# Performance work log

Measured on AMD Instinct MI355X. Metric: run time of the kernel, lower is better.

## Reference

```python
import jax, jax.numpy as jnp
import numpy as np


def _up(x, h, w):
    # bicubic (Keys a=-0.5, matching PIL BICUBIC) resize of [B,H,W] -> [B,h,w]
    return jax.image.resize(x, (x.shape[0], h, w), method='cubic')


def setup_inputs() -> dict:
    key = jax.random.key(0)
    ks = jax.random.split(key, 10)
    B = 64
    inp = {
        'cam_256': jax.random.uniform(ks[0], (B, 256, 256), dtype=jnp.float32),
        'cam_128': jax.random.uniform(ks[1], (B, 128, 128), dtype=jnp.float32),
        'cam_64':  jax.random.uniform(ks[2], (B, 64, 64), dtype=jnp.float32),
        'cam_32':  jax.random.uniform(ks[3], (B, 32, 32), dtype=jnp.float32),
        'w1': jax.random.normal(ks[4], (2,), dtype=jnp.float32),
        'b1': jax.random.normal(ks[5], (1,), dtype=jnp.float32),
        'w2': jax.random.normal(ks[6], (2,), dtype=jnp.float32),
        'b2': jax.random.normal(ks[7], (1,), dtype=jnp.float32),
        'w3': jax.random.normal(ks[8], (2,), dtype=jnp.float32),
        'b3': jax.random.normal(ks[9], (1,), dtype=jnp.float32),
    }
    return inp


def reference(cam_256, cam_128, cam_64, cam_32, w1, b1, w2, b2, w3, b3):
    B = cam_32.shape[0]
    # stage 1: up(32->64), concat with cam_64, 1x1 conv(2->1) + ReLU
    up32 = _up(cam_32, 64, 64)                              # [B,64,64]
    h64 = jax.nn.relu(w1[0] * up32 + w1[1] * cam_64 + b1[0])
    # stage 2: up(64->128), concat with cam_128, 1x1 conv + ReLU
    up64 = _up(h64, 128, 128)
    h128 = jax.nn.relu(w2[0] * up64 + w2[1] * cam_128 + b2[0])
    # stage 3: up(128->256), concat with cam_256, 1x1 conv + ReLU
    up128 = _up(h128, 256, 256)
    h256 = jax.nn.relu(w3[0] * up128 + w3[1] * cam_256 + b3[0])
    # final: bicubic up to 1024; original loop prepends each new image,
    # reversing batch order -> replicate with flip
    out = _up(h256, 1024, 1024)                             # [B,1024,1024]
    out = jnp.flip(out, axis=0)[:, None]                    # [B,1,1024,1024]
    return out
```

## Files before the change

kernel.cpp:

```cpp
#include <hip/hip_runtime.h>

typedef float vfloat4 __attribute__((ext_vector_type(4)));

__device__ __forceinline__ int iclamp(int v, int lo, int hi) {
  return v < lo ? lo : (v > hi ? hi : v);
}

__device__ __forceinline__ void taps4w(int i, int n, float inv, float w[4]) {
  float s = ((float)i + 0.5f) * inv - 0.5f;
  int k0 = (int)floorf(s);
  float sum = 0.f;
#pragma unroll
  for (int t = 0; t < 4; ++t) {
    int j = k0 - 1 + t;
    float d = fabsf(s - (float)j);
    float wt = (d <= 1.f) ? (((1.5f * d - 2.5f) * d) * d + 1.f)
                          : (((-0.5f * d + 2.5f) * d - 4.f) * d + 2.f);
    if (j < 0 || j >= n) wt = 0.f;
    w[t] = wt;
    sum += wt;
  }
  float r = 1.f / sum;
#pragma unroll
  for (int t = 0; t < 4; ++t) w[t] *= r;
}

#define W0_0 (-0.0439453125f)
#define W0_1 ( 0.3896484375f)
#define W0_2 ( 0.7275390625f)
#define W0_3 (-0.0732421875f)
#define W1_0 (-0.0068359375f)
#define W1_1 ( 0.0908203125f)
#define W1_2 ( 0.9638671875f)
#define W1_3 (-0.0478515625f)
#define U_0 (-0.0234375f)
#define U_1 ( 0.2265625f)
#define U_2 ( 0.8671875f)
#define U_3 (-0.0703125f)

__device__ __forceinline__ void up2_cell(const float (&f)[5][5], int k, int g, int n,
                                         float (&o)[2][2]) {
  if (g >= 2 && g <= n - 3 && k >= 2 && k <= n - 3) {
    float v0[5], v1[5];
#pragma unroll
    for (int c = 0; c < 5; ++c) {
      v0[c] = U_0 * f[0][c] + U_1 * f[1][c] + U_2 * f[2][c] + U_3 * f[3][c];
      v1[c] = U_3 * f[1][c] + U_2 * f[2][c] + U_1 * f[3][c] + U_0 * f[4][c];
    }
    o[0][0] = U_0 * v0[0] + U_1 * v0[1] + U_2 * v0[2] + U_3 * v0[3];
    o[0][1] = U_3 * v0[1] + U_2 * v0[2] + U_1 * v0[3] + U_0 * v0[4];
    o[1][0] = U_0 * v1[0] + U_1 * v1[1] + U_2 * v1[2] + U_3 * v1[3];
    o[1][1] = U_3 * v1[1] + U_2 * v1[2] + U_1 * v1[3] + U_0 * v1[4];
  } else {
#pragma unroll
    for (int p = 0; p < 2; ++p) {
      float wy[4];
      taps4w(2 * k + p, n, 0.5f, wy);
      float vv[5];
#pragma unroll
      for (int c = 0; c < 5; ++c)
        vv[c] = wy[0] * f[p][c] + wy[1] * f[p + 1][c] + wy[2] * f[p + 2][c] + wy[3] * f[p + 3][c];
#pragma unroll
      for (int q = 0; q < 2; ++q) {
        float wx[4];
        taps4w(2 * g + q, n, 0.5f, wx);
        o[p][q] = wx[0] * vv[q] + wx[1] * vv[q + 1] + wx[2] * vv[q + 2] + wx[3] * vv[q + 3];
      }
    }
  }
}

__device__ __forceinline__ void up4_cell(const float (&f)[5][5], int k, int g, int n,
                                         float (&o)[4][4]) {
  if (g >= 2 && g <= n - 3 && k >= 2 && k <= n - 3) {
    float vy[4][5];
#pragma unroll
    for (int c = 0; c < 5; ++c) {
      vy[0][c] = W0_0 * f[0][c] + W0_1 * f[1][c] + W0_2 * f[2][c] + W0_3 * f[3][c];
      vy[1][c] = W1_0 * f[0][c] + W1_1 * f[1][c] + W1_2 * f[2][c] + W1_3 * f[3][c];
      vy[2][c] = W1_3 * f[1][c] + W1_2 * f[2][c] + W1_1 * f[3][c] + W1_0 * f[4][c];
      vy[3][c] = W0_3 * f[1][c] + W0_2 * f[2][c] + W0_1 * f[3][c] + W0_0 * f[4][c];
    }
#pragma unroll
    for (int p = 0; p < 4; ++p) {
      o[p][0] = W0_0 * vy[p][0] + W0_1 * vy[p][1] + W0_2 * vy[p][2] + W0_3 * vy[p][3];
      o[p][1] = W1_0 * vy[p][0] + W1_1 * vy[p][1] + W1_2 * vy[p][2] + W1_3 * vy[p][3];
      o[p][2] = W1_3 * vy[p][1] + W1_2 * vy[p][2] + W1_1 * vy[p][3] + W1_0 * vy[p][4];
      o[p][3] = W0_3 * vy[p][1] + W0_2 * vy[p][2] + W0_1 * vy[p][3] + W0_0 * vy[p][4];
    }
  } else {
#pragma unroll
    for (int p = 0; p < 4; ++p) {
      float wy[4];
      taps4w(4 * k + p, n, 0.25f, wy);
      int oy = (p < 2) ? 0 : 1;
      float vv[5];
#pragma unroll
      for (int c = 0; c < 5; ++c)
        vv[c] = wy[0] * f[oy][c] + wy[1] * f[oy + 1][c] + wy[2] * f[oy + 2][c] + wy[3] * f[oy + 3][c];
#pragma unroll
      for (int q = 0; q < 4; ++q) {
        float wx[4];
        taps4w(4 * g + q, n, 0.25f, wx);
        int ox = (q < 2) ? 0 : 1;
        o[p][q] = wx[0] * vv[ox] + wx[1] * vv[ox + 1] + wx[2] * vv[ox + 2] + wx[3] * vv[ox + 3];
      }
    }
  }
}

__global__ void __launch_bounds__(512, 4) fused_all(
    const float* __restrict__ cam256, const float* __restrict__ cam128,
    const float* __restrict__ cam64, const float* __restrict__ cam32,
    const float* __restrict__ w1, const float* __restrict__ b1,
    const float* __restrict__ w2, const float* __restrict__ b2,
    const float* __restrict__ w3, const float* __restrict__ b3,
    float* __restrict__ out) {
  __shared__ float s_h64[16 * 64];
  __shared__ float s_h128[24 * 128];
  __shared__ float s_h256[36 * 256];

  const int tid = threadIdx.x;
  const int slab = blockIdx.x;
  const int b = blockIdx.y;
  const int s = slab * 32;

  const int r_lo = s - 2 < 0 ? 0 : s - 2, r_hi = s + 33 > 255 ? 255 : s + 33;
  const int kr0 = r_lo >> 1, kr1 = r_hi >> 1;
  const int h256_row0 = 2 * kr0;
  const int j_lo = kr0 - 2 < 0 ? 0 : kr0 - 2, j_hi = kr1 + 2 > 127 ? 127 : kr1 + 2;
  const int kj0 = j_lo >> 1, kj1 = j_hi >> 1;
  const int h128_row0 = 2 * kj0;
  const int m_lo = kj0 - 2 < 0 ? 0 : kj0 - 2, m_hi = kj1 + 2 > 63 ? 63 : kj1 + 2;
  const int km0 = m_lo >> 1, km1 = m_hi >> 1;
  const int h64_row0 = 2 * km0;

  const float w1_0 = w1[0], w1_1 = w1[1], b1_0 = b1[0];
  const float w2_0 = w2[0], w2_1 = w2[1], b2_0 = b2[0];
  const float w3_0 = w3[0], w3_1 = w3[1], b3_0 = b3[0];

  {
    const float* c32 = cam32 + (size_t)b * 32 * 32;
    const float* c64 = cam64 + (size_t)b * 64 * 64;
    const int nk = km1 - km0 + 1;
    for (int idx = tid; idx < nk * 32; idx += 512) {
      int k = km0 + (idx >> 5), g = idx & 31;
      float f[5][5];
#pragma unroll
      for (int i = 0; i < 5; ++i) {
        int r = iclamp(k - 2 + i, 0, 31);
#pragma unroll
        for (int c = 0; c < 5; ++c) f[i][c] = c32[r * 32 + iclamp(g - 2 + c, 0, 31)];
      }
      float o[2][2];
      up2_cell(f, k, g, 32, o);
#pragma unroll
      for (int p = 0; p < 2; ++p)
#pragma unroll
        for (int q = 0; q < 2; ++q) {
          int row = 2 * k + p, col = 2 * g + q;
          float h = w1_0 * o[p][q] + w1_1 * c64[row * 64 + col] + b1_0;
          s_h64[(row - h64_row0) * 64 + col] = fmaxf(h, 0.f);
        }
    }
  }
  __syncthreads();

  {
    const float* c128 = cam128 + (size_t)b * 128 * 128;
    const int nk = kj1 - kj0 + 1;
    for (int idx = tid; idx < nk * 64; idx += 512) {
      int k = kj0 + (idx >> 6), g = idx & 63;
      float f[5][5];
#pragma unroll
      for (int i = 0; i < 5; ++i) {
        int r = iclamp(k - 2 + i, 0, 63) - h64_row0;
#pragma unroll
        for (int c = 0; c < 5; ++c) f[i][c] = s_h64[r * 64 + iclamp(g - 2 + c, 0, 63)];
      }
      float o[2][2];
      up2_cell(f, k, g, 64, o);
#pragma unroll
      for (int p = 0; p < 2; ++p)
#pragma unroll
        for (int q = 0; q < 2; ++q) {
          int row = 2 * k + p, col = 2 * g + q;
          float h = w2_0 * o[p][q] + w2_1 * c128[row * 128 + col] + b2_0;
          s_h128[(row - h128_row0) * 128 + col] = fmaxf(h, 0.f);
        }
    }
  }
  __syncthreads();

  {
    const float* c256 = cam256 + (size_t)b * 256 * 256;
    const int nk = kr1 - kr0 + 1;
    for (int idx = tid; idx < nk * 128; idx += 512) {
      int k = kr0 + (idx >> 7), g = idx & 127;
      float f[5][5];
#pragma unroll
      for (int i = 0; i < 5; ++i) {
        int r = iclamp(k - 2 + i, 0, 127) - h128_row0;
#pragma unroll
        for (int c = 0; c < 5; ++c) f[i][c] = s_h128[r * 128 + iclamp(g - 2 + c, 0, 127)];
      }
      float o[2][2];
      up2_cell(f, k, g, 128, o);
#pragma unroll
      for (int p = 0; p < 2; ++p)
#pragma unroll
        for (int q = 0; q < 2; ++q) {
          int row = 2 * k + p, col = 2 * g + q;
          float h = w3_0 * o[p][q] + w3_1 * c256[row * 256 + col] + b3_0;
          s_h256[(row - h256_row0) * 256 + col] = fmaxf(h, 0.f);
        }
    }
  }
  __syncthreads();

  {
    float* outimg = out + (size_t)(63 - b) * 1024 * 1024;
    for (int idx = tid; idx < 32 * 256; idx += 512) {
      int k = s + (idx >> 8), g = idx & 255;
      float f[5][5];
#pragma unroll
      for (int i = 0; i < 5; ++i) {
        int r = iclamp(k - 2 + i, 0, 255) - h256_row0;
#pragma unroll
        for (int c = 0; c < 5; ++c) f[i][c] = s_h256[r * 256 + iclamp(g - 2 + c, 0, 255)];
      }
      float o[4][4];
      up4_cell(f, k, g, 256, o);
#pragma unroll
      for (int p = 0; p < 4; ++p) {
        vfloat4 v = {o[p][0], o[p][1], o[p][2], o[p][3]};
        __builtin_nontemporal_store(v, (vfloat4*)(outimg + (size_t)(4 * k + p) * 1024 + 4 * g));
      }
    }
  }
}

extern "C" void kernel_launch(void* const* d_in, const int* in_sizes, int n_in_,
                              void* d_out, int out_size, void* d_ws, size_t ws_size,
                              hipStream_t stream) {
  const float* cam256 = (const float*)d_in[0];
  const float* cam128 = (const float*)d_in[1];
  const float* cam64  = (const float*)d_in[2];
  const float* cam32  = (const float*)d_in[3];
  const float* w1 = (const float*)d_in[4];
  const float* b1 = (const float*)d_in[5];
  const float* w2 = (const float*)d_in[6];
  const float* b2 = (const float*)d_in[7];
  const float* w3 = (const float*)d_in[8];
  const float* b3 = (const float*)d_in[9];
  float* out = (float*)d_out;

  fused_all<<<dim3(8, 64), 512, 0, stream>>>(cam256, cam128, cam64, cam32,
                                             w1, b1, w2, b2, w3, b3, out);
}
```

Measured before the change: 334.5 us.

## Use sliding-window separable passes with register reuse in final two upsample stages

Stage 3 and the final 4x upsample now give each thread a fixed column and a run of consecutive rows. Each new row's horizontal filter result is kept in a 5-row register window that shifts down one row per step, so every shared-memory row is loaded and filtered horizontally once rather than five times. Column tap weights are computed once per thread, and stage 3 uses float2 loads and stores. The trade-off is more registers per thread and serial per-thread row loops, which may lower occupancy or reduce parallelism.

```diff
diff --git a/kernel.cpp b/kernel.cpp
--- a/kernel.cpp
+++ b/kernel.cpp
@@ -1,6 +1,7 @@
 #include <hip/hip_runtime.h>
 
 typedef float vfloat4 __attribute__((ext_vector_type(4)));
+typedef float vfloat2 __attribute__((ext_vector_type(2)));
 
 __device__ __forceinline__ int iclamp(int v, int lo, int hi) {
   return v < lo ? lo : (v > hi ? hi : v);
@@ -70,45 +71,6 @@
   }
 }
 
-__device__ __forceinline__ void up4_cell(const float (&f)[5][5], int k, int g, int n,
-                                         float (&o)[4][4]) {
-  if (g >= 2 && g <= n - 3 && k >= 2 && k <= n - 3) {
-    float vy[4][5];
-#pragma unroll
-    for (int c = 0; c < 5; ++c) {
-      vy[0][c] = W0_0 * f[0][c] + W0_1 * f[1][c] + W0_2 * f[2][c] + W0_3 * f[3][c];
-      vy[1][c] = W1_0 * f[0][c] + W1_1 * f[1][c] + W1_2 * f[2][c] + W1_3 * f[3][c];
-      vy[2][c] = W1_3 * f[1][c] + W1_2 * f[2][c] + W1_1 * f[3][c] + W1_0 * f[4][c];
-      vy[3][c] = W0_3 * f[1][c] + W0_2 * f[2][c] + W0_1 * f[3][c] + W0_0 * f[4][c];
-    }
-#pragma unroll
-    for (int p = 0; p < 4; ++p) {
-      o[p][0] = W0_0 * vy[p][0] + W0_1 * vy[p][1] + W0_2 * vy[p][2] + W0_3 * vy[p][3];
-      o[p][1] = W1_0 * vy[p][0] + W1_1 * vy[p][1] + W1_2 * vy[p][2] + W1_3 * vy[p][3];
-      o[p][2] = W1_3 * vy[p][1] + W1_2 * vy[p][2] + W1_1 * vy[p][3] + W1_0 * vy[p][4];
-      o[p][3] = W0_3 * vy[p][1] + W0_2 * vy[p][2] + W0_1 * vy[p][3] + W0_0 * vy[p][4];
-    }
-  } else {
-#pragma unroll
-    for (int p = 0; p < 4; ++p) {
-      float wy[4];
-      taps4w(4 * k + p, n, 0.25f, wy);
-      int oy = (p < 2) ? 0 : 1;
-      float vv[5];
-#pragma unroll
-      for (int c = 0; c < 5; ++c)
-        vv[c] = wy[0] * f[oy][c] + wy[1] * f[oy + 1][c] + wy[2] * f[oy + 2][c] + wy[3] * f[oy + 3][c];
-#pragma unroll
-      for (int q = 0; q < 4; ++q) {
-        float wx[4];
-        taps4w(4 * g + q, n, 0.25f, wx);
-        int ox = (q < 2) ? 0 : 1;
-        o[p][q] = wx[0] * vv[ox] + wx[1] * vv[ox + 1] + wx[2] * vv[ox + 2] + wx[3] * vv[ox + 3];
-      }
-    }
-  }
-}
-
 __global__ void __launch_bounds__(512, 4) fused_all(
     const float* __restrict__ cam256, const float* __restrict__ cam128,
     const float* __restrict__ cam64, const float* __restrict__ cam32,
@@ -194,49 +156,155 @@
 
   {
     const float* c256 = cam256 + (size_t)b * 256 * 256;
+    const int gc = tid & 127;
+    const int sub = tid >> 7;
     const int nk = kr1 - kr0 + 1;
-    for (int idx = tid; idx < nk * 128; idx += 512) {
-      int k = kr0 + (idx >> 7), g = idx & 127;
-      float f[5][5];
-#pragma unroll
-      for (int i = 0; i < 5; ++i) {
-        int r = iclamp(k - 2 + i, 0, 127) - h128_row0;
-#pragma unroll
-        for (int c = 0; c < 5; ++c) f[i][c] = s_h128[r * 128 + iclamp(g - 2 + c, 0, 127)];
-      }
-      float o[2][2];
-      up2_cell(f, k, g, 128, o);
-#pragma unroll
-      for (int p = 0; p < 2; ++p)
-#pragma unroll
-        for (int q = 0; q < 2; ++q) {
-          int row = 2 * k + p, col = 2 * g + q;
-          float h = w3_0 * o[p][q] + w3_1 * c256[row * 256 + col] + b3_0;
-          s_h256[(row - h256_row0) * 256 + col] = fmaxf(h, 0.f);
+    const int len = (nk + 3) >> 2;
+    const int ks = kr0 + sub * len;
+    int ke = ks + len - 1;
+    if (ke > kr1) ke = kr1;
+    if (ks <= kr1) {
+      const int cc0 = iclamp(gc - 2, 0, 127), cc1 = iclamp(gc - 1, 0, 127), cc2 = gc,
+                cc3 = iclamp(gc + 1, 0, 127), cc4 = iclamp(gc + 2, 0, 127);
+      float wa0, wa1, wa2, wa3, wb0, wb1, wb2, wb3;
+      if (gc >= 2 && gc <= 125) {
+        wa0 = U_0; wa1 = U_1; wa2 = U_2; wa3 = U_3;
+        wb0 = U_3; wb1 = U_2; wb2 = U_1; wb3 = U_0;
+      } else {
+        float ta[4], tb[4];
+        taps4w(2 * gc, 128, 0.5f, ta);
+        taps4w(2 * gc + 1, 128, 0.5f, tb);
+        wa0 = ta[0]; wa1 = ta[1]; wa2 = ta[2]; wa3 = ta[3];
+        wb0 = tb[0]; wb1 = tb[1]; wb2 = tb[2]; wb3 = tb[3];
+      }
+#define H128_ROW_HX(RCLAMP, DST)                                                \
+      {                                                                         \
+        const float* rp_ = s_h128 + ((RCLAMP) - h128_row0) * 128;               \
+        float f0_ = rp_[cc0], f1_ = rp_[cc1], f2_ = rp_[cc2], f3_ = rp_[cc3],   \
+              f4_ = rp_[cc4];                                                   \
+        DST[0] = wa0 * f0_ + wa1 * f1_ + wa2 * f2_ + wa3 * f3_;                 \
+        DST[1] = wb0 * f1_ + wb1 * f2_ + wb2 * f3_ + wb3 * f4_;                 \
+      }
+      float hx[5][2];
+#pragma unroll
+      for (int w = 0; w < 5; ++w) {
+        int rc = iclamp(ks - 2 + w, 0, 127);
+        H128_ROW_HX(rc, hx[w]);
+      }
+      for (int k = ks; k <= ke; ++k) {
+        if (k > ks) {
+#pragma unroll
+          for (int w = 0; w < 4; ++w) { hx[w][0] = hx[w + 1][0]; hx[w][1] = hx[w + 1][1]; }
+          int rc = iclamp(k + 2, 0, 127);
+          H128_ROW_HX(rc, hx[4]);
         }
+        float p0w[4], p1w[4];
+        if (k < 2 || k > 125) {
+          taps4w(2 * k, 128, 0.5f, p0w);
+          taps4w(2 * k + 1, 128, 0.5f, p1w);
+        } else {
+          p0w[0] = U_0; p0w[1] = U_1; p0w[2] = U_2; p0w[3] = U_3;
+          p1w[0] = U_3; p1w[1] = U_2; p1w[2] = U_1; p1w[3] = U_0;
+        }
+        float o00 = p0w[0] * hx[0][0] + p0w[1] * hx[1][0] + p0w[2] * hx[2][0] + p0w[3] * hx[3][0];
+        float o01 = p0w[0] * hx[0][1] + p0w[1] * hx[1][1] + p0w[2] * hx[2][1] + p0w[3] * hx[3][1];
+        float o10 = p1w[0] * hx[1][0] + p1w[1] * hx[2][0] + p1w[2] * hx[3][0] + p1w[3] * hx[4][0];
+        float o11 = p1w[0] * hx[1][1] + p1w[1] * hx[2][1] + p1w[2] * hx[3][1] + p1w[3] * hx[4][1];
+        const int row0 = 2 * k, col = 2 * gc;
+        vfloat2 ca = *(const vfloat2*)(c256 + (size_t)row0 * 256 + col);
+        vfloat2 cb = *(const vfloat2*)(c256 + (size_t)(row0 + 1) * 256 + col);
+        vfloat2 h0 = {fmaxf(w3_0 * o00 + w3_1 * ca.x + b3_0, 0.f),
+                      fmaxf(w3_0 * o01 + w3_1 * ca.y + b3_0, 0.f)};
+        vfloat2 h1 = {fmaxf(w3_0 * o10 + w3_1 * cb.x + b3_0, 0.f),
+                      fmaxf(w3_0 * o11 + w3_1 * cb.y + b3_0, 0.f)};
+        *(vfloat2*)(&s_h256[(row0 - h256_row0) * 256 + col]) = h0;
+        *(vfloat2*)(&s_h256[(row0 + 1 - h256_row0) * 256 + col]) = h1;
+      }
+#undef H128_ROW_HX
     }
   }
   __syncthreads();
 
   {
     float* outimg = out + (size_t)(63 - b) * 1024 * 1024;
-    for (int idx = tid; idx < 32 * 256; idx += 512) {
-      int k = s + (idx >> 8), g = idx & 255;
-      float f[5][5];
-#pragma unroll
-      for (int i = 0; i < 5; ++i) {
-        int r = iclamp(k - 2 + i, 0, 255) - h256_row0;
-#pragma unroll
-        for (int c = 0; c < 5; ++c) f[i][c] = s_h256[r * 256 + iclamp(g - 2 + c, 0, 255)];
-      }
-      float o[4][4];
-      up4_cell(f, k, g, 256, o);
-#pragma unroll
-      for (int p = 0; p < 4; ++p) {
-        vfloat4 v = {o[p][0], o[p][1], o[p][2], o[p][3]};
-        __builtin_nontemporal_store(v, (vfloat4*)(outimg + (size_t)(4 * k + p) * 1024 + 4 * g));
-      }
-    }
+    const int g = tid & 255;
+    const int kbase = s + (tid >> 8) * 16;
+    const int cc0 = iclamp(g - 2, 0, 255), cc1 = iclamp(g - 1, 0, 255), cc2 = g,
+              cc3 = iclamp(g + 1, 0, 255), cc4 = iclamp(g + 2, 0, 255);
+    float wx00, wx01, wx02, wx03, wx10, wx11, wx12, wx13;
+    float wx20, wx21, wx22, wx23, wx30, wx31, wx32, wx33;
+    if (g >= 2 && g <= 253) {
+      wx00 = W0_0; wx01 = W0_1; wx02 = W0_2; wx03 = W0_3;
+      wx10 = W1_0; wx11 = W1_1; wx12 = W1_2; wx13 = W1_3;
+      wx20 = W1_3; wx21 = W1_2; wx22 = W1_1; wx23 = W1_0;
+      wx30 = W0_3; wx31 = W0_2; wx32 = W0_1; wx33 = W0_0;
+    } else {
+      float t0[4], t1[4], t2[4], t3[4];
+      taps4w(4 * g + 0, 256, 0.25f, t0);
+      taps4w(4 * g + 1, 256, 0.25f, t1);
+      taps4w(4 * g + 2, 256, 0.25f, t2);
+      taps4w(4 * g + 3, 256, 0.25f, t3);
+      wx00 = t0[0]; wx01 = t0[1]; wx02 = t0[2]; wx03 = t0[3];
+      wx10 = t1[0]; wx11 = t1[1]; wx12 = t1[2]; wx13 = t1[3];
+      wx20 = t2[0]; wx21 = t2[1]; wx22 = t2[2]; wx23 = t2[3];
+      wx30 = t3[0]; wx31 = t3[1]; wx32 = t3[2]; wx33 = t3[3];
+    }
+#define H256_ROW_HX(RCLAMP, DST)                                                \
+    {                                                                           \
+      const float* rp_ = s_h256 + ((RCLAMP) - h256_row0) * 256;                 \
+      float f0_ = rp_[cc0], f1_ = rp_[cc1], f2_ = rp_[cc2], f3_ = rp_[cc3],     \
+            f4_ = rp_[cc4];                                                     \
+      DST[0] = wx00 * f0_ + wx01 * f1_ + wx02 * f2_ + wx03 * f3_;               \
+      DST[1] = wx10 * f0_ + wx11 * f1_ + wx12 * f2_ + wx13 * f3_;               \
+      DST[2] = wx20 * f1_ + wx21 * f2_ + wx22 * f3_ + wx23 * f4_;               \
+      DST[3] = wx30 * f1_ + wx31 * f2_ + wx32 * f3_ + wx33 * f4_;               \
+    }
+    float hx[5][4];
+#pragma unroll
+    for (int w = 0; w < 5; ++w) {
+      int rc = iclamp(kbase - 2 + w, 0, 255);
+      H256_ROW_HX(rc, hx[w]);
+    }
+    float* op = outimg + (size_t)4 * kbase * 1024 + 4 * g;
+#pragma unroll
+    for (int step = 0; step < 16; ++step) {
+      const int k = kbase + step;
+      if (step) {
+#pragma unroll
+        for (int w = 0; w < 4; ++w)
+#pragma unroll
+          for (int q = 0; q < 4; ++q) hx[w][q] = hx[w + 1][q];
+        int rc = iclamp(k + 2, 0, 255);
+        H256_ROW_HX(rc, hx[4]);
+      }
+      float wy0[4], wy1[4], wy2[4], wy3[4];
+      const bool maybe_bnd = (step < 2) || (step >= 14);
+      if (maybe_bnd && (k < 2 || k > 253)) {
+        taps4w(4 * k + 0, 256, 0.25f, wy0);
+        taps4w(4 * k + 1, 256, 0.25f, wy1);
+        taps4w(4 * k + 2, 256, 0.25f, wy2);
+        taps4w(4 * k + 3, 256, 0.25f, wy3);
+      } else {
+        wy0[0] = W0_0; wy0[1] = W0_1; wy0[2] = W0_2; wy0[3] = W0_3;
+        wy1[0] = W1_0; wy1[1] = W1_1; wy1[2] = W1_2; wy1[3] = W1_3;
+        wy2[0] = W1_3; wy2[1] = W1_2; wy2[2] = W1_1; wy2[3] = W1_0;
+        wy3[0] = W0_3; wy3[1] = W0_2; wy3[2] = W0_1; wy3[3] = W0_0;
+      }
+      vfloat4 v0, v1, v2, v3;
+#pragma unroll
+      for (int q = 0; q < 4; ++q) {
+        v0[q] = wy0[0] * hx[0][q] + wy0[1] * hx[1][q] + wy0[2] * hx[2][q] + wy0[3] * hx[3][q];
+        v1[q] = wy1[0] * hx[0][q] + wy1[1] * hx[1][q] + wy1[2] * hx[2][q] + wy1[3] * hx[3][q];
+        v2[q] = wy2[0] * hx[1][q] + wy2[1] * hx[2][q] + wy2[2] * hx[3][q] + wy2[3] * hx[4][q];
+        v3[q] = wy3[0] * hx[1][q] + wy3[1] * hx[2][q] + wy3[2] * hx[3][q] + wy3[3] * hx[4][q];
+      }
+      float* rp = op + (size_t)step * 4096;
+      __builtin_nontemporal_store(v0, (vfloat4*)(rp));
+      __builtin_nontemporal_store(v1, (vfloat4*)(rp + 1024));
+      __builtin_nontemporal_store(v2, (vfloat4*)(rp + 2048));
+      __builtin_nontemporal_store(v3, (vfloat4*)(rp + 3072));
+    }
+#undef H256_ROW_HX
   }
 }
 
```

Measured after the change: 303.3 us. -9.3%, faster.
